# Kernel optimization log

Hardware: AMD Instinct MI355X
Metric: run time of the kernel (lower is better)

Reference implementation:

```python
import jax, jax.numpy as jnp
import numpy as np


def setup_inputs() -> dict:
    key = jax.random.key(0)
    k1, k2, k3, k4 = jax.random.split(key, 4)
    B, T, d_model, d_internal = 4, 2048, 1024, 64
    x = jax.random.normal(k1, (B, T, d_model), dtype=jnp.float32)
    # torch.nn.Linear weights: [out_features, in_features]
    s = 1.0 / np.sqrt(d_model)
    W_Q = jax.random.uniform(k2, (d_internal, d_model), jnp.float32, -s, s)
    W_K = jax.random.uniform(k3, (d_internal, d_model), jnp.float32, -s, s)
    W_V = jax.random.uniform(k4, (d_internal, d_model), jnp.float32, -s, s)
    return {"x": x, "W_Q": W_Q, "W_K": W_K, "W_V": W_V}


def reference(x, W_Q, W_K, W_V):
    B, T, C = x.shape  # C == d_model
    Q = jnp.einsum('btc,dc->btd', x, W_Q)
    K = jnp.einsum('btc,dc->btd', x, W_K)
    # Faithful to source bug: V is computed with W_K, W_V is unused.
    V = jnp.einsum('btc,dc->btd', x, W_K)
    scale = C ** (-0.5)  # source scales by d_model, not d_internal
    attn = jnp.einsum('btd,bsd->bts', Q, K) * scale  # [B,T,T]
    causal = jnp.tril(jnp.ones((T, T), dtype=bool))
    attn = jnp.where(causal[None, :, :], attn, -jnp.inf)
    attn = jax.nn.softmax(attn, axis=-1)
    return jnp.einsum('bts,bsd->btd', attn, V)
```

## Files before the change

### kernel.cpp

```cpp
#include <hip/hip_runtime.h>
#include <hip/hip_bf16.h>
#include <cstdint>
#include <cstddef>

#define BB 4
#define TT 2048
#define DM 1024
#define DH 64
#define NCH 4

typedef __attribute__((ext_vector_type(8))) short short8;
typedef __attribute__((ext_vector_type(4))) float floatx4;

__device__ __forceinline__ unsigned short f2bf(float f) {
    union { float f; unsigned int u; } v; v.f = f;
    unsigned int u = v.u;
    u += 0x7fffu + ((u >> 16) & 1u);
    return (unsigned short)(u >> 16);
}

__device__ __forceinline__ float bf2f(unsigned short h) {
    union { unsigned int u; float f; } v;
    v.u = ((unsigned int)h) << 16;
    return v.f;
}

__device__ __forceinline__ unsigned int cvtpk(float a, float b) {
    unsigned int r;
    asm("v_cvt_pk_bf16_f32 %0, %1, %2" : "=v"(r) : "v"(a), "v"(b));
    return r;
}

__device__ __forceinline__ short8 cvt8(float4 lo, float4 hi) {
    union { unsigned int u[4]; short8 s; } v;
    v.u[0] = cvtpk(lo.x, lo.y);
    v.u[1] = cvtpk(lo.z, lo.w);
    v.u[2] = cvtpk(hi.x, hi.y);
    v.u[3] = cvtpk(hi.z, hi.w);
    return v.s;
}

#define WTHREADS (8 * 32 * 64)

__global__ __launch_bounds__(256) void wtile_kernel(const float* __restrict__ wq,
                                                    const float* __restrict__ wk,
                                                    unsigned short* __restrict__ wbt) {
    const int j  = blockIdx.x * 256 + threadIdx.x;
    const int l  = j & 63;
    const int kc = (j >> 6) & 31;
    const int nt = j >> 11;
    const float* wbase = (nt < 4) ? wq : wk;
    const float* src = wbase + (size_t)((nt & 3) * 16 + (l & 15)) * DM
                             + kc * 32 + (l >> 4) * 8;
    float4 a = *reinterpret_cast<const float4*>(src);
    float4 b = *reinterpret_cast<const float4*>(src + 4);
    *reinterpret_cast<short8*>(wbt + (size_t)j * 8) = cvt8(a, b);
}

__global__ __launch_bounds__(256) void proj_kernel(const float* __restrict__ x,
                                                   const unsigned short* __restrict__ wbt,
                                                   unsigned short* __restrict__ qo,
                                                   unsigned short* __restrict__ ko,
                                                   unsigned short* __restrict__ kt) {
    __shared__ __align__(16) unsigned short sA[2][16 * 64 * 8];

    const int tid  = threadIdx.x;
    const int wave = tid >> 6;
    const int lane = tid & 63;
    const int col  = lane & 15;
    const int quad = lane >> 4;
    const int mt   = blockIdx.x;

    const float* xtile = x + (size_t)mt * 16 * DM;
    const unsigned short* bq = wbt + ((size_t)wave * 32 * 64) * 8;
    const unsigned short* bk = wbt + ((size_t)(4 + wave) * 32 * 64) * 8;

    floatx4 accQ = (floatx4){0.f, 0.f, 0.f, 0.f};
    floatx4 accK = (floatx4){0.f, 0.f, 0.f, 0.f};

#pragma unroll 4
    for (int i = 0; i < 4; ++i) {
        const int e  = tid + i * 256;
        const int kc = e >> 6;
        const int l  = e & 63;
        const float* src = xtile + (size_t)(l & 15) * DM + kc * 32 + (l >> 4) * 8;
        float4 a = *reinterpret_cast<const float4*>(src);
        float4 b = *reinterpret_cast<const float4*>(src + 4);
        *reinterpret_cast<short8*>(sA[0] + (size_t)e * 8) = cvt8(a, b);
    }
    __syncthreads();

    float4 h1a[4], h1b[4];
#pragma unroll 4
    for (int i = 0; i < 4; ++i) {
        const int e  = tid + i * 256;
        const int kc = 16 + (e >> 6);
        const int l  = e & 63;
        const float* src = xtile + (size_t)(l & 15) * DM + kc * 32 + (l >> 4) * 8;
        h1a[i] = *reinterpret_cast<const float4*>(src);
        h1b[i] = *reinterpret_cast<const float4*>(src + 4);
    }

#pragma unroll
    for (int kc = 0; kc < 16; ++kc) {
        short8 a  = *reinterpret_cast<const short8*>(sA[0] + ((size_t)kc * 64 + lane) * 8);
        short8 b0 = *reinterpret_cast<const short8*>(bq + ((size_t)kc * 64 + lane) * 8);
        short8 b1 = *reinterpret_cast<const short8*>(bk + ((size_t)kc * 64 + lane) * 8);
        accQ = __builtin_amdgcn_mfma_f32_16x16x32_bf16(a, b0, accQ, 0, 0, 0);
        accK = __builtin_amdgcn_mfma_f32_16x16x32_bf16(a, b1, accK, 0, 0, 0);
    }

#pragma unroll 4
    for (int i = 0; i < 4; ++i) {
        const int e = tid + i * 256;
        *reinterpret_cast<short8*>(sA[1] + (size_t)e * 8) = cvt8(h1a[i], h1b[i]);
    }
    __syncthreads();

#pragma unroll
    for (int kc = 0; kc < 16; ++kc) {
        short8 a  = *reinterpret_cast<const short8*>(sA[1] + ((size_t)kc * 64 + lane) * 8);
        short8 b0 = *reinterpret_cast<const short8*>(bq + ((size_t)(16 + kc) * 64 + lane) * 8);
        short8 b1 = *reinterpret_cast<const short8*>(bk + ((size_t)(16 + kc) * 64 + lane) * 8);
        accQ = __builtin_amdgcn_mfma_f32_16x16x32_bf16(a, b0, accQ, 0, 0, 0);
        accK = __builtin_amdgcn_mfma_f32_16x16x32_bf16(a, b1, accK, 0, 0, 0);
    }

    const int g = wave * 16 + col;
    unsigned short hk[4];
#pragma unroll
    for (int r = 0; r < 4; ++r) {
        const size_t row = (size_t)(mt * 16 + quad * 4 + r);
        qo[row * DH + g] = f2bf(accQ[r] * 0.04508422f);
        hk[r] = f2bf(accK[r]);
        ko[row * DH + g] = hk[r];
    }

    __syncthreads();
    unsigned short* kts = (unsigned short*)sA;
#pragma unroll
    for (int r = 0; r < 4; ++r)
        kts[g * 16 + quad * 4 + r] = hk[r];
    __syncthreads();
    if (tid < 128) {
        const int d  = tid >> 1;
        const int s8 = (tid & 1) * 8;
        const int b4 = mt >> 7;
        const int s0 = (mt & 127) * 16 + s8;
        short8 v = *reinterpret_cast<const short8*>(kts + d * 16 + s8);
        *reinterpret_cast<short8*>(kt + ((size_t)(b4 * 64 + d)) * TT + s0) = v;
    }
}

__global__ __launch_bounds__(512) void flash_kernel(const unsigned short* __restrict__ qb,
                                                    const unsigned short* __restrict__ kb,
                                                    const unsigned short* __restrict__ ktb,
                                                    float* __restrict__ out) {
    const int qt = blockIdx.x & 63;
    const int b  = blockIdx.x >> 6;

    __shared__ __align__(16) unsigned short Pl[8][4][16][40];
    __shared__ __align__(16) float Ored[NCH][32][68];
    __shared__ float lred[NCH][32];

    const int tid  = threadIdx.x;
    const int wv   = tid >> 6;
    const int c    = wv >> 1;
    const int h    = wv & 1;
    const int lane = tid & 63;
    const int col  = lane & 15;
    const int quad = lane >> 4;

    const int q0   = qt * 32;
    const int nch  = (qt >> 4) + 1;

    if (c < nch) {
        const int qrow  = q0 + h * 16;
        const int s_beg = c * 512;
        const int s_end = min(s_beg + 512, q0 + 32);

        const unsigned short* qp  = qb  + ((size_t)b * TT + qrow) * DH;
        const unsigned short* kp  = kb  + (size_t)b * TT * DH;
        const unsigned short* ktp = ktb + (size_t)b * 64 * TT;

        short8 qf0 = *reinterpret_cast<const short8*>(qp + (size_t)col * DH + quad * 8);
        short8 qf1 = *reinterpret_cast<const short8*>(qp + (size_t)col * DH + 32 + quad * 8);

        floatx4 o[4];
#pragma unroll
        for (int t = 0; t < 4; ++t) o[t] = (floatx4){0.f, 0.f, 0.f, 0.f};
        float lrow[4] = {0.f, 0.f, 0.f, 0.f};
        int   myq[4];
#pragma unroll
        for (int r = 0; r < 4; ++r) myq[r] = qrow + quad * 4 + r;

        auto body = [&](int s0, int slot, bool domask) {
            float sv[2][4];
#pragma unroll
            for (int st = 0; st < 2; ++st) {
                const int skey = s0 + 2 * col + st;
                const unsigned short* kr = kp + (size_t)skey * DH + quad * 8;
                short8 kf0 = *reinterpret_cast<const short8*>(kr);
                short8 kf1 = *reinterpret_cast<const short8*>(kr + 32);
                floatx4 z = (floatx4){0.f, 0.f, 0.f, 0.f};
                z = __builtin_amdgcn_mfma_f32_16x16x32_bf16(qf0, kf0, z, 0, 0, 0);
                z = __builtin_amdgcn_mfma_f32_16x16x32_bf16(qf1, kf1, z, 0, 0, 0);
#pragma unroll
                for (int r = 0; r < 4; ++r) {
                    float p = __builtin_exp2f(z[r]);
                    if (domask) p = (skey <= myq[r]) ? p : 0.f;
                    sv[st][r] = p;
                    lrow[r] += p;
                }
            }
#pragma unroll
            for (int r = 0; r < 4; ++r) {
                unsigned int* prow = reinterpret_cast<unsigned int*>(&Pl[wv][slot][quad * 4 + r][0]);
                prow[col] = cvtpk(sv[0][r], sv[1][r]);
            }
            short8 pf = *reinterpret_cast<const short8*>(&Pl[wv][slot][col][quad * 8]);

#pragma unroll
            for (int t = 0; t < 4; ++t) {
                short8 vf = *reinterpret_cast<const short8*>(
                    ktp + (size_t)(t * 16 + col) * TT + s0 + quad * 8);
                o[t] = __builtin_amdgcn_mfma_f32_16x16x32_bf16(pf, vf, o[t], 0, 0, 0);
            }
        };

        const int nIter = (s_end - s_beg) >> 5;
#pragma unroll 4
        for (int i = 0; i < nIter; ++i) {
            const int s0 = s_beg + 32 * i;
            body(s0, i & 3, s0 == q0);
        }

#pragma unroll
        for (int m = 1; m < 16; m <<= 1)
#pragma unroll
            for (int r = 0; r < 4; ++r)
                lrow[r] += __shfl_xor(lrow[r], m, 64);

#pragma unroll
        for (int t = 0; t < 4; ++t)
#pragma unroll
            for (int r = 0; r < 4; ++r)
                Ored[c][h * 16 + quad * 4 + r][t * 16 + col] = o[t][r];
        if (col == 0) {
#pragma unroll
            for (int r = 0; r < 4; ++r)
                lred[c][h * 16 + quad * 4 + r] = lrow[r];
        }
    }
    __syncthreads();

    {
        const int row = tid >> 4;
        const int c4  = (tid & 15) * 4;
        float L = 0.f, a0 = 0.f, a1 = 0.f, a2 = 0.f, a3 = 0.f;
#pragma unroll
        for (int cc = 0; cc < NCH; ++cc) {
            if (cc >= nch) break;
            L  += lred[cc][row];
            a0 += Ored[cc][row][c4 + 0];
            a1 += Ored[cc][row][c4 + 1];
            a2 += Ored[cc][row][c4 + 2];
            a3 += Ored[cc][row][c4 + 3];
        }
        const float inv = 1.0f / L;
        float4 r = {a0 * inv, a1 * inv, a2 * inv, a3 * inv};
        *reinterpret_cast<float4*>(out + ((size_t)b * TT + q0 + row) * DH + c4) = r;
    }
}

extern "C" void kernel_launch(void* const* d_in, const int* in_sizes, int n_in,
                              void* d_out, int out_size, void* d_ws, size_t ws_size,
                              hipStream_t stream) {
    const float* x  = (const float*)d_in[0];
    const float* wq = (const float*)d_in[1];
    const float* wk = (const float*)d_in[2];

    unsigned short* wbt = (unsigned short*)d_ws;
    unsigned short* qo  = wbt + (size_t)WTHREADS * 8;
    unsigned short* ko  = qo + (size_t)BB * TT * DH;
    unsigned short* kt  = ko + (size_t)BB * TT * DH;
    float* out = (float*)d_out;

    hipLaunchKernelGGL(wtile_kernel, dim3(WTHREADS / 256), dim3(256), 0, stream, wq, wk, wbt);
    hipLaunchKernelGGL(proj_kernel,  dim3((BB * TT) / 16), dim3(256), 0, stream, x, wbt, qo, ko, kt);
    hipLaunchKernelGGL(flash_kernel, dim3(BB * 64),        dim3(512), 0, stream, qo, ko, kt, out);
}
```

Baseline: 117.6 us.

## Balance causal flash attention by pairing query tiles and splitting key range evenly

Each block now handles one 16-row half of two mirrored query tiles (p and 63-p), giving every block 65 key chunks in total. The eight waves split those chunks evenly, and partial outputs and row sums are merged with LDS atomics. This removes the load imbalance of the old per-query-tile scheme, where many waves sat idle on early tiles and chunk lengths varied. In exchange it adds zeroing, shared-memory atomic reductions, and two Q fragment sets held in registers.

Result: no change. 116.7 us (-0.8%).

```diff
diff --git a/kernel.cpp b/kernel.cpp
--- a/kernel.cpp
+++ b/kernel.cpp
@@ -7,7 +7,6 @@
 #define TT 2048
 #define DM 1024
 #define DH 64
-#define NCH 4
 
 typedef __attribute__((ext_vector_type(8))) short short8;
 typedef __attribute__((ext_vector_type(4))) float floatx4;
@@ -156,120 +155,135 @@
                                                     const unsigned short* __restrict__ kb,
                                                     const unsigned short* __restrict__ ktb,
                                                     float* __restrict__ out) {
-    const int qt = blockIdx.x & 63;
-    const int b  = blockIdx.x >> 6;
+    const int h = blockIdx.x & 1;
+    const int p = (blockIdx.x >> 1) & 31;
+    const int b = blockIdx.x >> 6;
+
+    const int qtA = p, qtB = 63 - p;
+    const int q0A = qtA * 32, q0B = qtB * 32;
 
     __shared__ __align__(16) unsigned short Pl[8][4][16][40];
-    __shared__ __align__(16) float Ored[NCH][32][68];
-    __shared__ float lred[NCH][32];
+    __shared__ __align__(16) float Ored[2][16][68];
+    __shared__ float lred[2][16];
 
     const int tid  = threadIdx.x;
     const int wv   = tid >> 6;
-    const int c    = wv >> 1;
-    const int h    = wv & 1;
     const int lane = tid & 63;
     const int col  = lane & 15;
     const int quad = lane >> 4;
 
-    const int q0   = qt * 32;
-    const int nch  = (qt >> 4) + 1;
-
-    if (c < nch) {
-        const int qrow  = q0 + h * 16;
-        const int s_beg = c * 512;
-        const int s_end = min(s_beg + 512, q0 + 32);
-
-        const unsigned short* qp  = qb  + ((size_t)b * TT + qrow) * DH;
-        const unsigned short* kp  = kb  + (size_t)b * TT * DH;
-        const unsigned short* ktp = ktb + (size_t)b * 64 * TT;
-
-        short8 qf0 = *reinterpret_cast<const short8*>(qp + (size_t)col * DH + quad * 8);
-        short8 qf1 = *reinterpret_cast<const short8*>(qp + (size_t)col * DH + 32 + quad * 8);
-
-        floatx4 o[4];
-#pragma unroll
-        for (int t = 0; t < 4; ++t) o[t] = (floatx4){0.f, 0.f, 0.f, 0.f};
-        float lrow[4] = {0.f, 0.f, 0.f, 0.f};
-        int   myq[4];
-#pragma unroll
-        for (int r = 0; r < 4; ++r) myq[r] = qrow + quad * 4 + r;
-
-        auto body = [&](int s0, int slot, bool domask) {
-            float sv[2][4];
-#pragma unroll
-            for (int st = 0; st < 2; ++st) {
-                const int skey = s0 + 2 * col + st;
-                const unsigned short* kr = kp + (size_t)skey * DH + quad * 8;
-                short8 kf0 = *reinterpret_cast<const short8*>(kr);
-                short8 kf1 = *reinterpret_cast<const short8*>(kr + 32);
-                floatx4 z = (floatx4){0.f, 0.f, 0.f, 0.f};
-                z = __builtin_amdgcn_mfma_f32_16x16x32_bf16(qf0, kf0, z, 0, 0, 0);
-                z = __builtin_amdgcn_mfma_f32_16x16x32_bf16(qf1, kf1, z, 0, 0, 0);
-#pragma unroll
-                for (int r = 0; r < 4; ++r) {
-                    float p = __builtin_exp2f(z[r]);
-                    if (domask) p = (skey <= myq[r]) ? p : 0.f;
-                    sv[st][r] = p;
-                    lrow[r] += p;
-                }
+    {
+        float* z = &Ored[0][0][0];
+        for (int i = tid; i < 2 * 16 * 68; i += 512) z[i] = 0.f;
+        if (tid < 32) lred[tid >> 4][tid & 15] = 0.f;
+    }
+    __syncthreads();
+
+    const unsigned short* kp  = kb  + (size_t)b * TT * DH;
+    const unsigned short* ktp = ktb + (size_t)b * 64 * TT;
+    const int qrowA = q0A + h * 16, qrowB = q0B + h * 16;
+    const unsigned short* qpA = qb + ((size_t)b * TT + qrowA) * DH;
+    const unsigned short* qpB = qb + ((size_t)b * TT + qrowB) * DH;
+
+    short8 qfA0 = *reinterpret_cast<const short8*>(qpA + (size_t)col * DH + quad * 8);
+    short8 qfA1 = *reinterpret_cast<const short8*>(qpA + (size_t)col * DH + 32 + quad * 8);
+    short8 qfB0 = *reinterpret_cast<const short8*>(qpB + (size_t)col * DH + quad * 8);
+    short8 qfB1 = *reinterpret_cast<const short8*>(qpB + (size_t)col * DH + 32 + quad * 8);
+
+    const int w0 = (65 * wv) >> 3;
+    const int w1 = (65 * (wv + 1)) >> 3;
+
+    floatx4 oA[4], oB[4];
+#pragma unroll
+    for (int t = 0; t < 4; ++t) { oA[t] = (floatx4){0.f,0.f,0.f,0.f}; oB[t] = (floatx4){0.f,0.f,0.f,0.f}; }
+    float lrowA[4] = {0.f,0.f,0.f,0.f}, lrowB[4] = {0.f,0.f,0.f,0.f};
+
+    auto body = [&](int s0, int slot, bool domask, const short8& qf0, const short8& qf1,
+                    int qrow, floatx4* o, float* lrow) {
+        float sv[2][4];
+#pragma unroll
+        for (int st = 0; st < 2; ++st) {
+            const int skey = s0 + 2 * col + st;
+            const unsigned short* kr = kp + (size_t)skey * DH + quad * 8;
+            short8 kf0 = *reinterpret_cast<const short8*>(kr);
+            short8 kf1 = *reinterpret_cast<const short8*>(kr + 32);
+            floatx4 z = (floatx4){0.f, 0.f, 0.f, 0.f};
+            z = __builtin_amdgcn_mfma_f32_16x16x32_bf16(qf0, kf0, z, 0, 0, 0);
+            z = __builtin_amdgcn_mfma_f32_16x16x32_bf16(qf1, kf1, z, 0, 0, 0);
+#pragma unroll
+            for (int r = 0; r < 4; ++r) {
+                float pv = __builtin_exp2f(z[r]);
+                if (domask) pv = (skey <= qrow + quad * 4 + r) ? pv : 0.f;
+                sv[st][r] = pv;
+                lrow[r] += pv;
             }
-#pragma unroll
-            for (int r = 0; r < 4; ++r) {
-                unsigned int* prow = reinterpret_cast<unsigned int*>(&Pl[wv][slot][quad * 4 + r][0]);
-                prow[col] = cvtpk(sv[0][r], sv[1][r]);
-            }
-            short8 pf = *reinterpret_cast<const short8*>(&Pl[wv][slot][col][quad * 8]);
-
-#pragma unroll
-            for (int t = 0; t < 4; ++t) {
-                short8 vf = *reinterpret_cast<const short8*>(
-                    ktp + (size_t)(t * 16 + col) * TT + s0 + quad * 8);
-                o[t] = __builtin_amdgcn_mfma_f32_16x16x32_bf16(pf, vf, o[t], 0, 0, 0);
-            }
-        };
-
-        const int nIter = (s_end - s_beg) >> 5;
-#pragma unroll 4
-        for (int i = 0; i < nIter; ++i) {
-            const int s0 = s_beg + 32 * i;
-            body(s0, i & 3, s0 == q0);
         }
-
-#pragma unroll
-        for (int m = 1; m < 16; m <<= 1)
+#pragma unroll
+        for (int r = 0; r < 4; ++r) {
+            unsigned int* prow = reinterpret_cast<unsigned int*>(&Pl[wv][slot][quad * 4 + r][0]);
+            prow[col] = cvtpk(sv[0][r], sv[1][r]);
+        }
+        short8 pf = *reinterpret_cast<const short8*>(&Pl[wv][slot][col][quad * 8]);
+
+#pragma unroll
+        for (int t = 0; t < 4; ++t) {
+            short8 vf = *reinterpret_cast<const short8*>(
+                ktp + (size_t)(t * 16 + col) * TT + s0 + quad * 8);
+            o[t] = __builtin_amdgcn_mfma_f32_16x16x32_bf16(pf, vf, o[t], 0, 0, 0);
+        }
+    };
+
+    const int a_end = min(w1, p + 1);
+    for (int j = w0; j < a_end; ++j)
+        body(32 * j, j & 3, j == qtA, qfA0, qfA1, qrowA, oA, lrowA);
+
+    const int b_beg = max(w0, p + 1);
+    for (int j = b_beg; j < w1; ++j) {
+        const int i = j - p - 1;
+        body(32 * i, j & 3, i == qtB, qfB0, qfB1, qrowB, oB, lrowB);
+    }
+
+#pragma unroll
+    for (int m = 1; m < 16; m <<= 1)
+#pragma unroll
+        for (int r = 0; r < 4; ++r) {
+            lrowA[r] += __shfl_xor(lrowA[r], m, 64);
+            lrowB[r] += __shfl_xor(lrowB[r], m, 64);
+        }
+
+    if (w0 < p + 1) {
+#pragma unroll
+        for (int t = 0; t < 4; ++t)
 #pragma unroll
             for (int r = 0; r < 4; ++r)
-                lrow[r] += __shfl_xor(lrow[r], m, 64);
-
+                atomicAdd(&Ored[0][quad * 4 + r][t * 16 + col], oA[t][r]);
+        if (col == 0)
+#pragma unroll
+            for (int r = 0; r < 4; ++r)
+                atomicAdd(&lred[0][quad * 4 + r], lrowA[r]);
+    }
+    if (w1 > p + 1) {
 #pragma unroll
         for (int t = 0; t < 4; ++t)
 #pragma unroll
             for (int r = 0; r < 4; ++r)
-                Ored[c][h * 16 + quad * 4 + r][t * 16 + col] = o[t][r];
-        if (col == 0) {
+                atomicAdd(&Ored[1][quad * 4 + r][t * 16 + col], oB[t][r]);
+        if (col == 0)
 #pragma unroll
             for (int r = 0; r < 4; ++r)
-                lred[c][h * 16 + quad * 4 + r] = lrow[r];
-        }
+                atomicAdd(&lred[1][quad * 4 + r], lrowB[r]);
     }
     __syncthreads();
 
     {
-        const int row = tid >> 4;
-        const int c4  = (tid & 15) * 4;
-        float L = 0.f, a0 = 0.f, a1 = 0.f, a2 = 0.f, a3 = 0.f;
-#pragma unroll
-        for (int cc = 0; cc < NCH; ++cc) {
-            if (cc >= nch) break;
-            L  += lred[cc][row];
-            a0 += Ored[cc][row][c4 + 0];
-            a1 += Ored[cc][row][c4 + 1];
-            a2 += Ored[cc][row][c4 + 2];
-            a3 += Ored[cc][row][c4 + 3];
-        }
-        const float inv = 1.0f / L;
-        float4 r = {a0 * inv, a1 * inv, a2 * inv, a3 * inv};
-        *reinterpret_cast<float4*>(out + ((size_t)b * TT + q0 + row) * DH + c4) = r;
+        const int tile = tid >> 8;
+        const int row  = (tid >> 4) & 15;
+        const int c4   = (tid & 15) * 4;
+        const float inv = 1.0f / lred[tile][row];
+        const int grow = (tile == 0 ? qrowA : qrowB) + row;
+        float4 r = {Ored[tile][row][c4 + 0] * inv, Ored[tile][row][c4 + 1] * inv,
+                    Ored[tile][row][c4 + 2] * inv, Ored[tile][row][c4 + 3] * inv};
+        *reinterpret_cast<float4*>(out + ((size_t)b * TT + grow) * DH + c4) = r;
     }
 }
 
```
